# Optimization experiments

Measured on AMD Instinct MI355X. Metric: run time of the kernel, lower is better.

The kernel has to match this reference:

```python
import jax, jax.numpy as jnp
import numpy as np

C = 64

def conv2d(x, w, b, pad):
    out = jax.lax.conv_general_dilated(x, w, (1, 1), [(pad, pad), (pad, pad)],
                                       dimension_numbers=('NCHW', 'OIHW', 'NCHW'))
    return out + b[None, :, None, None]


def deform_conv(x, w_off, b_off, w, b, pad):
    # Standard pure-pytorch DeformConv2d (offset conv is 3x3/pad1, sampling on
    # zero-padded input, p0 starts at 1, bilinear gather, then kxk weight contraction).
    ks = w.shape[-1]
    N = ks * ks
    B, Cc, H, W = x.shape
    off = conv2d(x, w_off, b_off, 1)                      # (B, 2N, H, W)
    xp = jnp.pad(x, ((0, 0), (0, 0), (pad, pad), (pad, pad))) if pad > 0 else x
    Hp, Wp = xp.shape[2], xp.shape[3]
    off = off.transpose(0, 2, 3, 1)                       # (B, H, W, 2N)
    r = jnp.arange(-(ks - 1) // 2, (ks - 1) // 2 + 1, dtype=x.dtype)
    pn_x = jnp.repeat(r, ks)                              # (N,) kernel row offsets (n = i*ks + j)
    pn_y = jnp.tile(r, ks)                                # (N,) kernel col offsets
    p0_x = jnp.arange(1, H + 1, dtype=x.dtype)[:, None, None]   # (H,1,1)
    p0_y = jnp.arange(1, W + 1, dtype=x.dtype)[:, None]         # (W,1)
    px = off[..., :N] + p0_x + pn_x                       # (B,H,W,N) sample rows
    py = off[..., N:] + p0_y + pn_y                       # (B,H,W,N) sample cols
    fx = jnp.floor(jax.lax.stop_gradient(px))
    fy = jnp.floor(jax.lax.stop_gradient(py))
    lt_x = jnp.clip(fx, 0, Hp - 1)
    lt_y = jnp.clip(fy, 0, Wp - 1)
    rb_x = jnp.clip(fx + 1, 0, Hp - 1)
    rb_y = jnp.clip(fy + 1, 0, Wp - 1)
    pxc = jnp.clip(px, 0, Hp - 1)
    pyc = jnp.clip(py, 0, Wp - 1)
    g_lt = (1 + (lt_x - pxc)) * (1 + (lt_y - pyc))
    g_rb = (1 - (rb_x - pxc)) * (1 - (rb_y - pyc))
    g_lb = (1 + (lt_x - pxc)) * (1 - (rb_y - pyc))
    g_rt = (1 - (rb_x - pxc)) * (1 + (lt_y - pyc))
    xpf = xp.reshape(B, Cc, Hp * Wp)

    def gather(qx, qy):
        idx = (qx * Wp + qy).astype(jnp.int32).reshape(B, 1, -1)
        g = jnp.take_along_axis(xpf, jnp.broadcast_to(idx, (B, Cc, idx.shape[-1])), axis=2)
        return g.reshape(B, Cc, H, W, N)

    x_off = (g_lt[:, None] * gather(lt_x, lt_y) +
             g_rb[:, None] * gather(rb_x, rb_y) +
             g_lb[:, None] * gather(lt_x, rb_y) +
             g_rt[:, None] * gather(rb_x, lt_y))          # (B,C,H,W,N)
    out = jnp.einsum('bchwn,ocn->bohw', x_off, w.reshape(w.shape[0], Cc, N))
    return out + b[None, :, None, None]


def setup_inputs() -> dict:
    key = jax.random.key(0)
    ks_list = [1, 3, 5]
    keys = jax.random.split(key, 32)
    inp = {'x': jax.random.normal(keys[0], (4, C, 96, 96), dtype=jnp.float32)}
    i = 1
    for ks in ks_list:
        N = ks * ks
        inp[f'wo{ks}'] = jax.random.normal(keys[i], (2 * N, C, 3, 3), dtype=jnp.float32) * 0.01; i += 1
        inp[f'bo{ks}'] = jax.random.normal(keys[i], (2 * N,), dtype=jnp.float32) * 0.01; i += 1
        inp[f'w{ks}'] = jax.random.normal(keys[i], (C, C, ks, ks), dtype=jnp.float32) * 0.05; i += 1
        inp[f'b{ks}'] = jax.random.normal(keys[i], (C,), dtype=jnp.float32) * 0.05; i += 1
        inp[f'wa{ks}'] = jax.random.normal(keys[i], (C, C, ks, ks), dtype=jnp.float32) * 0.05; i += 1
        inp[f'ba{ks}'] = jax.random.normal(keys[i], (C,), dtype=jnp.float32) * 0.05; i += 1
    return inp


def reference(x, wo1, bo1, w1, b1, wa1, ba1, wo3, bo3, w3, b3, wa3, ba3, wo5, bo5, w5, b5, wa5, ba5):
    lrelu = lambda t: jnp.where(t >= 0, t, 0.1 * t)
    x1 = lrelu(deform_conv(x, wo1, bo1, w1, b1, 0))
    x2 = lrelu(deform_conv(x, wo3, bo3, w3, b3, 1))
    x3 = lrelu(deform_conv(x, wo5, bo5, w5, b5, 2))
    msf = x1 + x2 + x3
    att = jax.nn.sigmoid(conv2d(msf, wa1, ba1, 0) + conv2d(msf, wa3, ba3, 1) + conv2d(msf, wa5, ba5, 2))
    return msf * att + msf
```

## Files before the change

kernel.cpp:

```cpp
#include <hip/hip_runtime.h>
#include <math.h>

constexpr int B = 4, C = 64, H = 96, W = 96, HW = H * W;

typedef __attribute__((ext_vector_type(8))) short bf16x8;
typedef __attribute__((ext_vector_type(4))) float f32x4;
typedef __attribute__((ext_vector_type(4))) unsigned int uint4v;

constexpr size_t OFF_OFFALL = 0;
constexpr size_t OFF_MSF    = OFF_OFFALL;
constexpr size_t OFF_X1     = OFF_OFFALL + (size_t)B*72*HW;
constexpr size_t OFF_X2     = OFF_X1  + (size_t)B*64*HW;
constexpr size_t OFF_X3A    = OFF_X2  + (size_t)B*64*HW;
constexpr size_t OFF_X3B    = OFF_X3A + (size_t)B*64*HW;
constexpr size_t OFF_X3C    = OFF_X3B + (size_t)B*64*HW;
constexpr size_t OFF_WOT    = OFF_X3C + (size_t)B*64*HW;
constexpr size_t OFF_BOALL  = OFF_WOT + (size_t)64*9*72;
constexpr size_t OFF_WPKH   = OFF_BOALL + 128;
constexpr size_t OFF_WPKL   = OFF_WPKH + 71680;
constexpr size_t OFF_WEFF   = OFF_WPKL + 71680;
constexpr size_t OFF_BEFF   = OFF_WEFF + (size_t)64*25*64;

__global__ void prep_all(const float* __restrict__ wo1, const float* __restrict__ bo1,
                         const float* __restrict__ wo3, const float* __restrict__ bo3,
                         const float* __restrict__ wo5, const float* __restrict__ bo5,
                         const float* __restrict__ w1, const float* __restrict__ w3,
                         const float* __restrict__ w5,
                         const float* __restrict__ wa1, const float* __restrict__ ba1,
                         const float* __restrict__ wa3, const float* __restrict__ ba3,
                         const float* __restrict__ wa5, const float* __restrict__ ba5,
                         float* __restrict__ woT, float* __restrict__ boAll,
                         unsigned short* __restrict__ wPkH, unsigned short* __restrict__ wPkL,
                         float* __restrict__ weff, float* __restrict__ beff) {
  int idx = blockIdx.x * 256 + threadIdx.x;
  if (idx < 41472) {
    int ic = idx / (9 * 72), tap = (idx / 72) % 9, oc = idx % 72;
    float v = 0.f;
    if (oc < 2)       v = wo1[(oc * 64 + ic) * 9 + tap];
    else if (oc < 20) v = wo3[((oc - 2) * 64 + ic) * 9 + tap];
    else if (oc < 70) v = wo5[((oc - 20) * 64 + ic) * 9 + tap];
    woT[idx] = v;
  }
  if (idx < 72) boAll[idx] = idx < 2 ? bo1[idx] : idx < 20 ? bo3[idx - 2] : idx < 70 ? bo5[idx - 20] : 0.f;
  if (idx < 64) beff[idx] = ba1[idx] + ba3[idx] + ba5[idx];
  int i3 = idx - 41472;
  if (i3 >= 0 && i3 < 102400) {
    int ic = i3 / 1600, tap = (i3 / 64) % 25, oc = i3 & 63;
    int kh = tap / 5, kw = tap % 5;
    float v = wa5[(oc * 64 + ic) * 25 + tap];
    if (kh >= 1 && kh <= 3 && kw >= 1 && kw <= 3)
      v += wa3[(oc * 64 + ic) * 9 + (kh - 1) * 3 + (kw - 1)];
    if (tap == 12) v += wa1[oc * 64 + ic];
    weff[i3] = v;
  }
  int e = idx - 143872;
  if (e >= 0 && e < 143360) {
    int i  = e & 7;
    int l  = (e >> 3) & 63;
    int nt = (e >> 9) & 3;
    int kt = (e >> 11) & 1;
    int tap = e >> 12;
    int c  = kt * 32 + 8 * (l >> 4) + i;
    int oc = nt * 16 + (l & 15);
    float w;
    if (tap == 0)      w = w1[oc * 64 + c];
    else if (tap < 10) w = w3[(oc * 64 + c) * 9 + (tap - 1)];
    else               w = w5[(oc * 64 + c) * 25 + (tap - 10)];
    unsigned bits = __float_as_uint(w);
    unsigned hib  = bits & 0xffff0000u;
    float lo = w - __uint_as_float(hib);
    wPkH[e] = (unsigned short)(bits >> 16);
    wPkL[e] = (unsigned short)(__float_as_uint(lo) >> 16);
  }
}

template <int NOC, int OCB>
__device__ __forceinline__ void conv_off_body(const float* __restrict__ x,
                                              const float* __restrict__ woT,
                                              const float* __restrict__ boAll,
                                              float* __restrict__ offAll,
                                              float* __restrict__ xs,
                                              float* __restrict__ wsh,
                                              int h, int b, int tid) {
  constexpr int OCPG = NOC / 8;
  const int ocg = tid >> 5, pixg = tid & 31;
  const int oc0 = ocg * OCPG, w0 = pixg * 3;
  float acc[OCPG][3] = {};

  for (int cc = 0; cc < 8; ++cc) {
    __syncthreads();
    for (int idx = tid; idx < 2400; idx += 256) {
      int ic = idx / 300, r = (idx / 100) % 3, j = idx % 100;
      int wc = j - 1, hr = h - 1 + r;
      float v = 0.f;
      if (wc >= 0 && wc < 96 && hr >= 0 && hr < 96)
        v = x[((size_t)(b * 64 + cc * 8 + ic) * 96 + hr) * 96 + wc];
      xs[(ic * 3 + r) * 100 + j] = v;
    }
    for (int i = tid; i < 8 * 9 * NOC; i += 256) {
      int ic = i / (9 * NOC), rem = i % (9 * NOC), tap = rem / NOC, j = rem % NOC;
      wsh[i] = woT[((size_t)(cc * 8 + ic) * 9 + tap) * 72 + OCB + j];
    }
    __syncthreads();
#pragma unroll 2
    for (int ic = 0; ic < 8; ++ic) {
#pragma unroll
      for (int kh = 0; kh < 3; ++kh) {
        float xv[5];
#pragma unroll
        for (int t = 0; t < 5; ++t) xv[t] = xs[(ic * 3 + kh) * 100 + w0 + t];
#pragma unroll
        for (int kw = 0; kw < 3; ++kw) {
          const float* wrow = &wsh[(ic * 9 + kh * 3 + kw) * NOC + oc0];
#pragma unroll
          for (int o = 0; o < OCPG; ++o) {
            float wv = wrow[o];
            acc[o][0] += wv * xv[kw + 0];
            acc[o][1] += wv * xv[kw + 1];
            acc[o][2] += wv * xv[kw + 2];
          }
        }
      }
    }
  }
#pragma unroll
  for (int o = 0; o < OCPG; ++o) {
    int oc = OCB + oc0 + o;
    float bias = boAll[oc];
#pragma unroll
    for (int p = 0; p < 3; ++p)
      offAll[((size_t)(b * 72 + oc) * 96 + h) * 96 + w0 + p] = acc[o][p] + bias;
  }
}

__global__ __launch_bounds__(256) void conv_off(const float* __restrict__ x,
                                                const float* __restrict__ woT,
                                                const float* __restrict__ boAll,
                                                float* __restrict__ offAll) {
  __shared__ __align__(16) float xs[8 * 3 * 100];
  __shared__ __align__(16) float wsh[8 * 9 * 40];
  const int bid = blockIdx.x, tid = threadIdx.x;
  const int r = bid & 7, q = bid >> 3;
  const int b = r >> 1, half = r & 1;
  const int z = q & 1, h = half * 48 + (q >> 1);
  if (z == 0) conv_off_body<40, 0>(x, woT, boAll, offAll, xs, wsh, h, b, tid);
  else        conv_off_body<32, 40>(x, woT, boAll, offAll, xs, wsh, h, b, tid);
}

template <int KS>
__device__ __forceinline__ void deform_mfma_body(const float* __restrict__ xb,
                                                 const float* __restrict__ offAll,
                                                 const unsigned short* __restrict__ wPkH,
                                                 const unsigned short* __restrict__ wPkL,
                                                 float* __restrict__ dst,
                                                 int n0, int n1, int b, int h0,
                                                 int* __restrict__ spb, int* __restrict__ spd,
                                                 float* __restrict__ spg, int tid) {
  constexpr int N = KS * KS, P = (KS - 1) / 2, HP = H + 2 * P;
  constexpr int CHB = KS == 1 ? 0 : KS == 3 ? 2 : 20;
  constexpr int GB  = KS == 1 ? 0 : KS == 3 ? 1 : 10;
  const int lane = tid & 63, wv = tid >> 6;
  const int pxw = wv * 48, lg = lane >> 4, lm = lane & 15;
  f32x4 acc[3][4];
#pragma unroll
  for (int a1 = 0; a1 < 3; ++a1)
#pragma unroll
    for (int a2 = 0; a2 < 4; ++a2) acc[a1][a2] = (f32x4)0.f;

  for (int n = n0; n < n1; ++n) {
    const int buf = n & 1;
    int* sb = spb + buf * 192;
    int* sd = spd + buf * 192;
    float* sg = spg + buf * 768;
    if (tid < 192) {
      int w = tid % 96, rr = tid / 96, h = h0 + rr;
      float ox = offAll[((size_t)(b * 72 + CHB + n) * 96 + h) * 96 + w];
      float oy = offAll[((size_t)(b * 72 + CHB + N + n) * 96 + h) * 96 + w];
      float pxf = ox + (float)(h + 1 + n / KS - P);
      float pyf = oy + (float)(w + 1 + n % KS - P);
      float fx = floorf(pxf), fy = floorf(pyf);
      float hpm = (float)(HP - 1);
      float ltx = fminf(fmaxf(fx, 0.f), hpm);
      float rbx = fminf(fmaxf(fx + 1.f, 0.f), hpm);
      float lty = fminf(fmaxf(fy, 0.f), hpm);
      float rby = fminf(fmaxf(fy + 1.f, 0.f), hpm);
      float pxc = fminf(fmaxf(pxf, 0.f), hpm);
      float pyc = fminf(fmaxf(pyf, 0.f), hpm);
      float gx0 = 1.f + (ltx - pxc);
      float gx1 = 1.f - (rbx - pxc);
      float gy0 = 1.f + (lty - pyc);
      float gy1 = 1.f - (rby - pyc);
      int rx0 = (int)ltx - P, rx1 = (int)rbx - P;
      int ry0 = (int)lty - P, ry1 = (int)rby - P;
      float vx0 = (rx0 >= 0 && rx0 < 96) ? 1.f : 0.f;
      float vx1 = (rx1 >= 0 && rx1 < 96) ? 1.f : 0.f;
      float vy0 = (ry0 >= 0 && ry0 < 96) ? 1.f : 0.f;
      float vy1 = (ry1 >= 0 && ry1 < 96) ? 1.f : 0.f;
      int cx0 = min(max(rx0, 0), 95), cx1 = min(max(rx1, 0), 95);
      int cy0 = min(max(ry0, 0), 95), cy1 = min(max(ry1, 0), 95);
      sb[tid] = cx0 * 96 + cy0;
      sd[tid] = (cx1 - cx0) * 96 | ((cy1 - cy0) << 16);
      sg[0 * 192 + tid] = gx0 * gy0 * vx0 * vy0;
      sg[1 * 192 + tid] = gx1 * gy1 * vx1 * vy1;
      sg[2 * 192 + tid] = gx0 * gy1 * vx0 * vy1;
      sg[3 * 192 + tid] = gx1 * gy0 * vx1 * vy0;
    }
    __syncthreads();
#pragma unroll
    for (int kt = 0; kt < 2; ++kt) {
      const int bb = (((GB + n) * 2 + kt)) * 256 + lane;
      uint4v bh[4], bl[4];
#pragma unroll
      for (int nt = 0; nt < 4; ++nt) {
        bh[nt] = reinterpret_cast<const uint4v*>(wPkH)[bb + nt * 64];
        bl[nt] = reinterpret_cast<const uint4v*>(wPkL)[bb + nt * 64];
      }
#pragma unroll
      for (int mt = 0; mt < 3; ++mt) {
        int px = pxw + mt * 16 + lm;
        int base = sb[px];
        int d = sd[px];
        int dx = d & 0xffff, dy = d >> 16;
        float g0 = sg[px], g1 = sg[192 + px], g2 = sg[384 + px], g3 = sg[576 + px];
        const float* xc = xb + (size_t)(kt * 32 + lg * 8) * HW + base;
        float vv[8];
#pragma unroll
        for (int i = 0; i < 8; ++i) {
          const float* p = xc + (size_t)i * HW;
          vv[i] = g0 * p[0] + g1 * p[dx + dy] + g2 * p[dy] + g3 * p[dx];
        }
        unsigned hp[4], lp[4];
#pragma unroll
        for (int j = 0; j < 4; ++j) {
          unsigned b0 = __float_as_uint(vv[2 * j]), b1 = __float_as_uint(vv[2 * j + 1]);
          unsigned h0b = b0 & 0xffff0000u, h1b = b1 & 0xffff0000u;
          float l0 = vv[2 * j] - __uint_as_float(h0b);
          float l1 = vv[2 * j + 1] - __uint_as_float(h1b);
          hp[j] = (b0 >> 16) | h1b;
          lp[j] = (__float_as_uint(l0) >> 16) | (__float_as_uint(l1) & 0xffff0000u);
        }
        uint4v hv = {hp[0], hp[1], hp[2], hp[3]};
        uint4v lv = {lp[0], lp[1], lp[2], lp[3]};
        bf16x8 ah = __builtin_bit_cast(bf16x8, hv);
        bf16x8 al = __builtin_bit_cast(bf16x8, lv);
#pragma unroll
        for (int nt = 0; nt < 4; ++nt) {
          bf16x8 BH = __builtin_bit_cast(bf16x8, bh[nt]);
          bf16x8 BL = __builtin_bit_cast(bf16x8, bl[nt]);
          acc[mt][nt] = __builtin_amdgcn_mfma_f32_16x16x32_bf16(ah, BH, acc[mt][nt], 0, 0, 0);
          acc[mt][nt] = __builtin_amdgcn_mfma_f32_16x16x32_bf16(al, BH, acc[mt][nt], 0, 0, 0);
          acc[mt][nt] = __builtin_amdgcn_mfma_f32_16x16x32_bf16(ah, BL, acc[mt][nt], 0, 0, 0);
        }
      }
    }
  }
#pragma unroll
  for (int mt = 0; mt < 3; ++mt) {
#pragma unroll
    for (int reg = 0; reg < 4; ++reg) {
      int px = pxw + mt * 16 + lg * 4 + reg;
      int rr = px >= 96 ? 1 : 0;
      int wcol = px - rr * 96;
#pragma unroll
      for (int nt = 0; nt < 4; ++nt) {
        int oc = nt * 16 + lm;
        dst[((size_t)(b * 64 + oc) * 96 + h0 + rr) * 96 + wcol] = acc[mt][nt][reg];
      }
    }
  }
}

__global__ __launch_bounds__(256, 3) void deform_mfma(const float* __restrict__ x,
                                                      const float* __restrict__ offAll,
                                                      const unsigned short* __restrict__ wPkH,
                                                      const unsigned short* __restrict__ wPkL,
                                                      float* __restrict__ x1,
                                                      float* __restrict__ x2,
                                                      float* __restrict__ x3a,
                                                      float* __restrict__ x3b,
                                                      float* __restrict__ x3c) {
  __shared__ int spb[2 * 192], spd[2 * 192];
  __shared__ float spg[2 * 768];
  const int bid = blockIdx.x, tid = threadIdx.x;
  const int r = bid & 7, q = bid >> 3;
  const int b = r >> 1, half = r & 1;
  const int typ = q & 3, strip = half * 24 + (q >> 2);
  const int h0 = strip * 2;
  const float* xb = x + (size_t)b * 64 * HW;
  if (typ == 0)
    deform_mfma_body<5>(xb, offAll, wPkH, wPkL, x3a, 0, 9, b, h0, spb, spd, spg, tid);
  else if (typ == 1)
    deform_mfma_body<5>(xb, offAll, wPkH, wPkL, x3b, 9, 17, b, h0, spb, spd, spg, tid);
  else if (typ == 2)
    deform_mfma_body<5>(xb, offAll, wPkH, wPkL, x3c, 17, 25, b, h0, spb, spd, spg, tid);
  else {
    deform_mfma_body<3>(xb, offAll, wPkH, wPkL, x2, 0, 9, b, h0, spb, spd, spg, tid);
    __syncthreads();
    deform_mfma_body<1>(xb, offAll, wPkH, wPkL, x1, 0, 1, b, h0, spb, spd, spg, tid);
  }
}

__global__ __launch_bounds__(256) void msf_build(const float* __restrict__ x1,
                                                 const float* __restrict__ x2,
                                                 const float* __restrict__ x3a,
                                                 const float* __restrict__ x3b,
                                                 const float* __restrict__ x3c,
                                                 const float* __restrict__ b1,
                                                 const float* __restrict__ b3,
                                                 const float* __restrict__ b5,
                                                 float* __restrict__ msf) {
  int i = blockIdx.x * 256 + threadIdx.x;
  int c = (i / 2304) & 63;
  float bb1 = b1[c], bb3 = b3[c], bb5 = b5[c];
  float4 v1 = reinterpret_cast<const float4*>(x1)[i];
  float4 v2 = reinterpret_cast<const float4*>(x2)[i];
  float4 va = reinterpret_cast<const float4*>(x3a)[i];
  float4 vb = reinterpret_cast<const float4*>(x3b)[i];
  float4 vc = reinterpret_cast<const float4*>(x3c)[i];
  float4 m;
  float a1, a2, a3;
  a1 = v1.x + bb1; a1 = a1 >= 0.f ? a1 : 0.1f * a1;
  a2 = v2.x + bb3; a2 = a2 >= 0.f ? a2 : 0.1f * a2;
  a3 = va.x + vb.x + vc.x + bb5; a3 = a3 >= 0.f ? a3 : 0.1f * a3;
  m.x = a1 + a2 + a3;
  a1 = v1.y + bb1; a1 = a1 >= 0.f ? a1 : 0.1f * a1;
  a2 = v2.y + bb3; a2 = a2 >= 0.f ? a2 : 0.1f * a2;
  a3 = va.y + vb.y + vc.y + bb5; a3 = a3 >= 0.f ? a3 : 0.1f * a3;
  m.y = a1 + a2 + a3;
  a1 = v1.z + bb1; a1 = a1 >= 0.f ? a1 : 0.1f * a1;
  a2 = v2.z + bb3; a2 = a2 >= 0.f ? a2 : 0.1f * a2;
  a3 = va.z + vb.z + vc.z + bb5; a3 = a3 >= 0.f ? a3 : 0.1f * a3;
  m.z = a1 + a2 + a3;
  a1 = v1.w + bb1; a1 = a1 >= 0.f ? a1 : 0.1f * a1;
  a2 = v2.w + bb3; a2 = a2 >= 0.f ? a2 : 0.1f * a2;
  a3 = va.w + vb.w + vc.w + bb5; a3 = a3 >= 0.f ? a3 : 0.1f * a3;
  m.w = a1 + a2 + a3;
  reinterpret_cast<float4*>(msf)[i] = m;
}

__global__ __launch_bounds__(256) void att_final(const float* __restrict__ msf,
                                                 const float* __restrict__ weff,
                                                 const float* __restrict__ beff,
                                                 float* __restrict__ out) {
  __shared__ __align__(16) float xs[4 * 5 * 100];
  __shared__ __align__(16) float wsh[4 * 25 * 32];
  const int bid = blockIdx.x, tid = threadIdx.x;
  const int r = bid & 7, q = bid >> 3;
  const int b = r >> 1, half = r & 1;
  const int zhalf = q & 1, h = half * 48 + (q >> 1);
  const int zoc = zhalf * 32;
  const int ocg = tid >> 5, colg = tid & 31;
  const int oc0 = ocg * 4, w0 = colg * 3;
  float acc[4][3] = {};

  for (int cc = 0; cc < 16; ++cc) {
    __syncthreads();
    for (int idx = tid; idx < 2000; idx += 256) {
      int ic = idx / 500, rr = (idx / 100) % 5, j = idx % 100;
      int hr = h - 2 + rr, wc = j - 2;
      float v = 0.f;
      if (hr >= 0 && hr < 96 && wc >= 0 && wc < 96)
        v = msf[((size_t)(b * 64 + cc * 4 + ic) * 96 + hr) * 96 + wc];
      xs[idx] = v;
    }
    for (int i = tid; i < 800; i += 256) {
      int ict = i >> 3, qq = i & 7;
      int ic = ict / 25, tap = ict % 25;
      reinterpret_cast<float4*>(wsh)[i] =
          *reinterpret_cast<const float4*>(weff + ((size_t)(cc * 4 + ic) * 25 + tap) * 64 + zoc + qq * 4);
    }
    __syncthreads();
#pragma unroll
    for (int ic = 0; ic < 4; ++ic) {
#pragma unroll
      for (int kh = 0; kh < 5; ++kh) {
        float xv[7];
#pragma unroll
        for (int t = 0; t < 7; ++t) xv[t] = xs[ic * 500 + kh * 100 + w0 + t];
#pragma unroll
        for (int kw = 0; kw < 5; ++kw) {
          const float4 wv = *reinterpret_cast<const float4*>(&wsh[(ic * 25 + kh * 5 + kw) * 32 + oc0]);
          float wvv[4] = {wv.x, wv.y, wv.z, wv.w};
#pragma unroll
          for (int o = 0; o < 4; ++o) {
            acc[o][0] += wvv[o] * xv[kw + 0];
            acc[o][1] += wvv[o] * xv[kw + 1];
            acc[o][2] += wvv[o] * xv[kw + 2];
          }
        }
      }
    }
  }
#pragma unroll
  for (int o = 0; o < 4; ++o) {
    int oc = zoc + oc0 + o;
    float bz = beff[oc];
#pragma unroll
    for (int p = 0; p < 3; ++p) {
      float z = acc[o][p] + bz;
      float att = 1.f / (1.f + __expf(-z));
      size_t oi = ((size_t)(b * 64 + oc) * 96 + h) * 96 + w0 + p;
      float m = msf[oi];
      out[oi] = m + m * att;
    }
  }
}

extern "C" void kernel_launch(void* const* d_in, const int* in_sizes, int n_in,
                              void* d_out, int out_size, void* d_ws, size_t ws_size,
                              hipStream_t stream) {
  const float* x   = (const float*)d_in[0];
  const float* wo1 = (const float*)d_in[1];
  const float* bo1 = (const float*)d_in[2];
  const float* w1  = (const float*)d_in[3];
  const float* b1  = (const float*)d_in[4];
  const float* wa1 = (const float*)d_in[5];
  const float* ba1 = (const float*)d_in[6];
  const float* wo3 = (const float*)d_in[7];
  const float* bo3 = (const float*)d_in[8];
  const float* w3  = (const float*)d_in[9];
  const float* b3  = (const float*)d_in[10];
  const float* wa3 = (const float*)d_in[11];
  const float* ba3 = (const float*)d_in[12];
  const float* wo5 = (const float*)d_in[13];
  const float* bo5 = (const float*)d_in[14];
  const float* w5  = (const float*)d_in[15];
  const float* b5  = (const float*)d_in[16];
  const float* wa5 = (const float*)d_in[17];
  const float* ba5 = (const float*)d_in[18];

  float* ws     = (float*)d_ws;
  float* offAll = ws + OFF_OFFALL;
  float* msf    = ws + OFF_MSF;
  float* x1     = ws + OFF_X1;
  float* x2     = ws + OFF_X2;
  float* x3a    = ws + OFF_X3A;
  float* x3b    = ws + OFF_X3B;
  float* x3c    = ws + OFF_X3C;
  float* woT    = ws + OFF_WOT;
  float* boAll  = ws + OFF_BOALL;
  unsigned short* wPkH = (unsigned short*)(ws + OFF_WPKH);
  unsigned short* wPkL = (unsigned short*)(ws + OFF_WPKL);
  float* weff   = ws + OFF_WEFF;
  float* beff   = ws + OFF_BEFF;

  float* out = (float*)d_out;

  hipLaunchKernelGGL(prep_all, dim3(1122), dim3(256), 0, stream,
                     wo1, bo1, wo3, bo3, wo5, bo5, w1, w3, w5,
                     wa1, ba1, wa3, ba3, wa5, ba5,
                     woT, boAll, wPkH, wPkL, weff, beff);
  hipLaunchKernelGGL(conv_off, dim3(768), dim3(256), 0, stream, x, woT, boAll, offAll);
  hipLaunchKernelGGL(deform_mfma, dim3(768), dim3(256), 0, stream,
                     x, offAll, wPkH, wPkL, x1, x2, x3a, x3b, x3c);
  hipLaunchKernelGGL(msf_build, dim3(2304), dim3(256), 0, stream,
                     x1, x2, x3a, x3b, x3c, b1, b3, b5, msf);
  hipLaunchKernelGGL(att_final, dim3(768), dim3(256), 0, stream,
                     msf, weff, beff, out);
}
```

Measured before the change: 609.8 us.

## Split deform tiles to one row per block with six waves

The deformable conv MFMA kernel now gives each block a single output row instead of two. It runs 384 threads (six waves, one 16-pixel M-tile each) instead of four waves with three M-tiles each, and the grid doubles to 1536 blocks. The goal is fewer accumulator registers per thread and higher occupancy to hide the latency of the bilinear gathers. In exchange, the B-operand weight fragments are reloaded per block with less reuse, and each block does half as much work against its sync and offset-setup overhead.

```diff
diff --git a/kernel.cpp b/kernel.cpp
--- a/kernel.cpp
+++ b/kernel.cpp
@@ -153,27 +153,25 @@
                                                  const unsigned short* __restrict__ wPkH,
                                                  const unsigned short* __restrict__ wPkL,
                                                  float* __restrict__ dst,
-                                                 int n0, int n1, int b, int h0,
+                                                 int n0, int n1, int b, int h,
                                                  int* __restrict__ spb, int* __restrict__ spd,
                                                  float* __restrict__ spg, int tid) {
   constexpr int N = KS * KS, P = (KS - 1) / 2, HP = H + 2 * P;
   constexpr int CHB = KS == 1 ? 0 : KS == 3 ? 2 : 20;
   constexpr int GB  = KS == 1 ? 0 : KS == 3 ? 1 : 10;
   const int lane = tid & 63, wv = tid >> 6;
-  const int pxw = wv * 48, lg = lane >> 4, lm = lane & 15;
-  f32x4 acc[3][4];
-#pragma unroll
-  for (int a1 = 0; a1 < 3; ++a1)
-#pragma unroll
-    for (int a2 = 0; a2 < 4; ++a2) acc[a1][a2] = (f32x4)0.f;
+  const int pxw = wv * 16, lg = lane >> 4, lm = lane & 15;
+  f32x4 acc[4];
+#pragma unroll
+  for (int a2 = 0; a2 < 4; ++a2) acc[a2] = (f32x4)0.f;
 
   for (int n = n0; n < n1; ++n) {
     const int buf = n & 1;
-    int* sb = spb + buf * 192;
-    int* sd = spd + buf * 192;
-    float* sg = spg + buf * 768;
-    if (tid < 192) {
-      int w = tid % 96, rr = tid / 96, h = h0 + rr;
+    int* sb = spb + buf * 96;
+    int* sd = spd + buf * 96;
+    float* sg = spg + buf * 384;
+    if (tid < 96) {
+      int w = tid;
       float ox = offAll[((size_t)(b * 72 + CHB + n) * 96 + h) * 96 + w];
       float oy = offAll[((size_t)(b * 72 + CHB + N + n) * 96 + h) * 96 + w];
       float pxf = ox + (float)(h + 1 + n / KS - P);
@@ -200,12 +198,17 @@
       int cy0 = min(max(ry0, 0), 95), cy1 = min(max(ry1, 0), 95);
       sb[tid] = cx0 * 96 + cy0;
       sd[tid] = (cx1 - cx0) * 96 | ((cy1 - cy0) << 16);
-      sg[0 * 192 + tid] = gx0 * gy0 * vx0 * vy0;
-      sg[1 * 192 + tid] = gx1 * gy1 * vx1 * vy1;
-      sg[2 * 192 + tid] = gx0 * gy1 * vx0 * vy1;
-      sg[3 * 192 + tid] = gx1 * gy0 * vx1 * vy0;
-    }
-    __syncthreads();
+      sg[0 * 96 + tid] = gx0 * gy0 * vx0 * vy0;
+      sg[1 * 96 + tid] = gx1 * gy1 * vx1 * vy1;
+      sg[2 * 96 + tid] = gx0 * gy1 * vx0 * vy1;
+      sg[3 * 96 + tid] = gx1 * gy0 * vx1 * vy0;
+    }
+    __syncthreads();
+    const int px = pxw + lm;
+    const int base = sb[px];
+    const int d = sd[px];
+    const int dx = d & 0xffff, dy = d >> 16;
+    const float g0 = sg[px], g1 = sg[96 + px], g2 = sg[192 + px], g3 = sg[288 + px];
 #pragma unroll
     for (int kt = 0; kt < 2; ++kt) {
       const int bb = (((GB + n) * 2 + kt)) * 256 + lane;
@@ -215,62 +218,49 @@
         bh[nt] = reinterpret_cast<const uint4v*>(wPkH)[bb + nt * 64];
         bl[nt] = reinterpret_cast<const uint4v*>(wPkL)[bb + nt * 64];
       }
-#pragma unroll
-      for (int mt = 0; mt < 3; ++mt) {
-        int px = pxw + mt * 16 + lm;
-        int base = sb[px];
-        int d = sd[px];
-        int dx = d & 0xffff, dy = d >> 16;
-        float g0 = sg[px], g1 = sg[192 + px], g2 = sg[384 + px], g3 = sg[576 + px];
-        const float* xc = xb + (size_t)(kt * 32 + lg * 8) * HW + base;
-        float vv[8];
-#pragma unroll
-        for (int i = 0; i < 8; ++i) {
-          const float* p = xc + (size_t)i * HW;
-          vv[i] = g0 * p[0] + g1 * p[dx + dy] + g2 * p[dy] + g3 * p[dx];
-        }
-        unsigned hp[4], lp[4];
-#pragma unroll
-        for (int j = 0; j < 4; ++j) {
-          unsigned b0 = __float_as_uint(vv[2 * j]), b1 = __float_as_uint(vv[2 * j + 1]);
-          unsigned h0b = b0 & 0xffff0000u, h1b = b1 & 0xffff0000u;
-          float l0 = vv[2 * j] - __uint_as_float(h0b);
-          float l1 = vv[2 * j + 1] - __uint_as_float(h1b);
-          hp[j] = (b0 >> 16) | h1b;
-          lp[j] = (__float_as_uint(l0) >> 16) | (__float_as_uint(l1) & 0xffff0000u);
-        }
-        uint4v hv = {hp[0], hp[1], hp[2], hp[3]};
-        uint4v lv = {lp[0], lp[1], lp[2], lp[3]};
-        bf16x8 ah = __builtin_bit_cast(bf16x8, hv);
-        bf16x8 al = __builtin_bit_cast(bf16x8, lv);
-#pragma unroll
-        for (int nt = 0; nt < 4; ++nt) {
-          bf16x8 BH = __builtin_bit_cast(bf16x8, bh[nt]);
-          bf16x8 BL = __builtin_bit_cast(bf16x8, bl[nt]);
-          acc[mt][nt] = __builtin_amdgcn_mfma_f32_16x16x32_bf16(ah, BH, acc[mt][nt], 0, 0, 0);
-          acc[mt][nt] = __builtin_amdgcn_mfma_f32_16x16x32_bf16(al, BH, acc[mt][nt], 0, 0, 0);
-          acc[mt][nt] = __builtin_amdgcn_mfma_f32_16x16x32_bf16(ah, BL, acc[mt][nt], 0, 0, 0);
-        }
-      }
-    }
-  }
-#pragma unroll
-  for (int mt = 0; mt < 3; ++mt) {
-#pragma unroll
-    for (int reg = 0; reg < 4; ++reg) {
-      int px = pxw + mt * 16 + lg * 4 + reg;
-      int rr = px >= 96 ? 1 : 0;
-      int wcol = px - rr * 96;
+      const float* xc = xb + (size_t)(kt * 32 + lg * 8) * HW + base;
+      float vv[8];
+#pragma unroll
+      for (int i = 0; i < 8; ++i) {
+        const float* p = xc + (size_t)i * HW;
+        vv[i] = g0 * p[0] + g1 * p[dx + dy] + g2 * p[dy] + g3 * p[dx];
+      }
+      unsigned hp[4], lp[4];
+#pragma unroll
+      for (int j = 0; j < 4; ++j) {
+        unsigned b0 = __float_as_uint(vv[2 * j]), b1 = __float_as_uint(vv[2 * j + 1]);
+        unsigned h0b = b0 & 0xffff0000u, h1b = b1 & 0xffff0000u;
+        float l0 = vv[2 * j] - __uint_as_float(h0b);
+        float l1 = vv[2 * j + 1] - __uint_as_float(h1b);
+        hp[j] = (b0 >> 16) | h1b;
+        lp[j] = (__float_as_uint(l0) >> 16) | (__float_as_uint(l1) & 0xffff0000u);
+      }
+      uint4v hv = {hp[0], hp[1], hp[2], hp[3]};
+      uint4v lv = {lp[0], lp[1], lp[2], lp[3]};
+      bf16x8 ah = __builtin_bit_cast(bf16x8, hv);
+      bf16x8 al = __builtin_bit_cast(bf16x8, lv);
 #pragma unroll
       for (int nt = 0; nt < 4; ++nt) {
-        int oc = nt * 16 + lm;
-        dst[((size_t)(b * 64 + oc) * 96 + h0 + rr) * 96 + wcol] = acc[mt][nt][reg];
-      }
-    }
-  }
-}
-
-__global__ __launch_bounds__(256, 3) void deform_mfma(const float* __restrict__ x,
+        bf16x8 BH = __builtin_bit_cast(bf16x8, bh[nt]);
+        bf16x8 BL = __builtin_bit_cast(bf16x8, bl[nt]);
+        acc[nt] = __builtin_amdgcn_mfma_f32_16x16x32_bf16(ah, BH, acc[nt], 0, 0, 0);
+        acc[nt] = __builtin_amdgcn_mfma_f32_16x16x32_bf16(al, BH, acc[nt], 0, 0, 0);
+        acc[nt] = __builtin_amdgcn_mfma_f32_16x16x32_bf16(ah, BL, acc[nt], 0, 0, 0);
+      }
+    }
+  }
+#pragma unroll
+  for (int reg = 0; reg < 4; ++reg) {
+    int wcol = pxw + lg * 4 + reg;
+#pragma unroll
+    for (int nt = 0; nt < 4; ++nt) {
+      int oc = nt * 16 + lm;
+      dst[((size_t)(b * 64 + oc) * 96 + h) * 96 + wcol] = acc[nt][reg];
+    }
+  }
+}
+
+__global__ __launch_bounds__(384, 6) void deform_mfma(const float* __restrict__ x,
                                                       const float* __restrict__ offAll,
                                                       const unsigned short* __restrict__ wPkH,
                                                       const unsigned short* __restrict__ wPkL,
@@ -279,24 +269,24 @@
                                                       float* __restrict__ x3a,
                                                       float* __restrict__ x3b,
                                                       float* __restrict__ x3c) {
-  __shared__ int spb[2 * 192], spd[2 * 192];
-  __shared__ float spg[2 * 768];
+  __shared__ int spb[2 * 96], spd[2 * 96];
+  __shared__ float spg[2 * 384];
   const int bid = blockIdx.x, tid = threadIdx.x;
   const int r = bid & 7, q = bid >> 3;
   const int b = r >> 1, half = r & 1;
-  const int typ = q & 3, strip = half * 24 + (q >> 2);
-  const int h0 = strip * 2;
+  const int typ = q & 3, hh = q >> 2;
+  const int h = half * 48 + hh;
   const float* xb = x + (size_t)b * 64 * HW;
   if (typ == 0)
-    deform_mfma_body<5>(xb, offAll, wPkH, wPkL, x3a, 0, 9, b, h0, spb, spd, spg, tid);
+    deform_mfma_body<5>(xb, offAll, wPkH, wPkL, x3a, 0, 9, b, h, spb, spd, spg, tid);
   else if (typ == 1)
-    deform_mfma_body<5>(xb, offAll, wPkH, wPkL, x3b, 9, 17, b, h0, spb, spd, spg, tid);
+    deform_mfma_body<5>(xb, offAll, wPkH, wPkL, x3b, 9, 17, b, h, spb, spd, spg, tid);
   else if (typ == 2)
-    deform_mfma_body<5>(xb, offAll, wPkH, wPkL, x3c, 17, 25, b, h0, spb, spd, spg, tid);
+    deform_mfma_body<5>(xb, offAll, wPkH, wPkL, x3c, 17, 25, b, h, spb, spd, spg, tid);
   else {
-    deform_mfma_body<3>(xb, offAll, wPkH, wPkL, x2, 0, 9, b, h0, spb, spd, spg, tid);
-    __syncthreads();
-    deform_mfma_body<1>(xb, offAll, wPkH, wPkL, x1, 0, 1, b, h0, spb, spd, spg, tid);
+    deform_mfma_body<3>(xb, offAll, wPkH, wPkL, x2, 0, 9, b, h, spb, spd, spg, tid);
+    __syncthreads();
+    deform_mfma_body<1>(xb, offAll, wPkH, wPkL, x1, 0, 1, b, h, spb, spd, spg, tid);
   }
 }
 
@@ -451,7 +441,7 @@
                      wa1, ba1, wa3, ba3, wa5, ba5,
                      woT, boAll, wPkH, wPkL, weff, beff);
   hipLaunchKernelGGL(conv_off, dim3(768), dim3(256), 0, stream, x, woT, boAll, offAll);
-  hipLaunchKernelGGL(deform_mfma, dim3(768), dim3(256), 0, stream,
+  hipLaunchKernelGGL(deform_mfma, dim3(1536), dim3(384), 0, stream,
                      x, offAll, wPkH, wPkL, x1, x2, x3a, x3b, x3c);
   hipLaunchKernelGGL(msf_build, dim3(2304), dim3(256), 0, stream,
                      x1, x2, x3a, x3b, x3c, b1, b3, b5, msf);
```

Result: slower. 662.4 us (+8.6%).
